# Performance work log

Hardware: AMD Instinct MI355X
Metric: run time of the kernel (lower is better)

The kernel has to match this reference:

```python
import jax, jax.numpy as jnp
import numpy as np

NEG = -1.0e9


def setup_inputs() -> dict:
    key = jax.random.key(0)
    ks = jax.random.split(key, 8)
    B, L, D = 4, 2048, 1024
    s = 1.0 / np.sqrt(D)
    return {
        "x": jax.random.normal(ks[0], (B, L, D), dtype=jnp.float32),
        "Wq": jax.random.normal(ks[1], (D, D), dtype=jnp.float32) * s,
        "bq": jax.random.normal(ks[2], (D,), dtype=jnp.float32) * 0.02,
        "Wk": jax.random.normal(ks[3], (D, D), dtype=jnp.float32) * s,
        "bk": jax.random.normal(ks[4], (D,), dtype=jnp.float32) * 0.02,
        "Wv": jax.random.normal(ks[5], (D, D), dtype=jnp.float32) * s,
        "bv": jax.random.normal(ks[6], (D,), dtype=jnp.float32) * 0.02,
        "lengths": jax.random.randint(ks[7], (B,), 1, 2048, dtype=jnp.int32),
    }


def reference(x, Wq, bq, Wk, bk, Wv, bv, lengths):
    # x: [B, L, D]; single-head self-attention with causal + length additive masks
    B, L, D = x.shape
    q = x @ Wq + bq  # [B, L, D]
    k = x @ Wk + bk
    v = x @ Wv + bv
    scale = 1.0 / jnp.sqrt(jnp.asarray(D, dtype=x.dtype))
    att = jnp.einsum("bid,bjd->bij", q, k) * scale  # [B, L, L]
    idx = jnp.arange(L)
    causal = jnp.where(idx[None, :] > idx[:, None], NEG, 0.0).astype(x.dtype)  # [L, L]
    # length mask: NEG where j >= len[b] or i >= len[b]
    invalid = (idx[None, :] >= lengths[:, None])  # [B, L]
    lenmask = jnp.where(invalid[:, :, None] | invalid[:, None, :], NEG, 0.0).astype(x.dtype)
    att = att + causal[None, :, :] + lenmask
    att = jax.nn.softmax(att, axis=-1)
    return jnp.einsum("bij,bjd->bid", att, v)
```

## Files before the change

kernel.cpp:

```cpp
#include <hip/hip_runtime.h>

#define NEGV (-1.0e9f)

typedef __bf16 bf16_t;
typedef __bf16 bf16x8 __attribute__((ext_vector_type(8)));
typedef __bf16 bf16x4 __attribute__((ext_vector_type(4)));
typedef float  f32x4  __attribute__((ext_vector_type(4)));

__device__ __forceinline__ void gld16(const void* g, void* l) {
    __builtin_amdgcn_global_load_lds(
        (const __attribute__((address_space(1))) void*)g,
        (__attribute__((address_space(3))) void*)l, 16, 0, 0);
}


#define STG(P0, P1, BASE, NB, HOFS) do {               \
    gld16(P0, (BASE) + (NB) * 32768 + (HOFS));         \
    gld16(P1, (BASE) + (NB) * 32768 + (HOFS) + 8192);  \
    P0 += 64; P1 += 64; } while (0)

#define MMROW(ai)                                                                                    \
    acc[ib + ai][0] = __builtin_amdgcn_mfma_f32_16x16x32_bf16(a##ai, b0, acc[ib + ai][0], 0, 0, 0);  \
    acc[ib + ai][1] = __builtin_amdgcn_mfma_f32_16x16x32_bf16(a##ai, b1, acc[ib + ai][1], 0, 0, 0);  \
    acc[ib + ai][2] = __builtin_amdgcn_mfma_f32_16x16x32_bf16(a##ai, b2, acc[ib + ai][2], 0, 0, 0);  \
    acc[ib + ai][3] = __builtin_amdgcn_mfma_f32_16x16x32_bf16(a##ai, b3, acc[ib + ai][3], 0, 0, 0)

#define PHASE(BUFO, HOFS, PK, STAGE_STMT, ENDW) do {                     \
    bf16x8 a0 = *(const bf16x8*)(rdA + (BUFO) + (HOFS)        + (PK));   \
    bf16x8 a1 = *(const bf16x8*)(rdA + (BUFO) + (HOFS) + 2048 + (PK));   \
    bf16x8 a2 = *(const bf16x8*)(rdA + (BUFO) + (HOFS) + 4096 + (PK));   \
    bf16x8 a3 = *(const bf16x8*)(rdA + (BUFO) + (HOFS) + 6144 + (PK));   \
    bf16x8 b0 = *(const bf16x8*)(rdB + (BUFO)          + (PK));          \
    bf16x8 b1 = *(const bf16x8*)(rdB + (BUFO) + 2048   + (PK));          \
    bf16x8 b2 = *(const bf16x8*)(rdB + (BUFO) + 4096   + (PK));          \
    bf16x8 b3 = *(const bf16x8*)(rdB + (BUFO) + 6144   + (PK));          \
    STAGE_STMT;                                                          \
    __builtin_amdgcn_s_barrier();                                        \
    asm volatile("s_waitcnt lgkmcnt(0)" ::: "memory");                   \
    __builtin_amdgcn_s_setprio(1);                                       \
    {                                                                    \
        const int ib = (HOFS) ? 4 : 0;                                   \
        MMROW(0); MMROW(1); MMROW(2); MMROW(3);                          \
    }                                                                    \
    __builtin_amdgcn_s_setprio(0);                                       \
    ENDW;                                                                \
    __builtin_amdgcn_s_barrier();                                        \
} while (0)

__device__ __forceinline__ void mainloop256(
    const bf16_t* __restrict__ A, const bf16_t* __restrict__ B,
    int ldA, int ldB, int nkt, char* smem, int tid, f32x4 acc[8][4])
{
    const int w    = tid >> 6;
    const int lane = tid & 63;
    const int wm   = w & 1;
    const int wn   = w >> 1;
    const int l16  = lane & 15;
    const int quad = lane >> 4;

    const int r0 = tid >> 3;
    const int c0 = ((tid & 7) ^ (r0 & 7)) * 8;
    const int s1 = 512 + tid;
    const int r1 = s1 >> 3;
    const int c1 = ((s1 & 7) ^ (r1 & 7)) * 8;

    const bf16_t* pa00 = A + (size_t)(r0)       * ldA + c0;
    const bf16_t* pa01 = A + (size_t)(r1)       * ldA + c1;
    const bf16_t* pa10 = A + (size_t)(128 + r0) * ldA + c0;
    const bf16_t* pa11 = A + (size_t)(128 + r1) * ldA + c1;
    const bf16_t* pb00 = B + (size_t)(r0)       * ldB + c0;
    const bf16_t* pb01 = B + (size_t)(r1)       * ldB + c1;
    const bf16_t* pb10 = B + (size_t)(128 + r0) * ldB + c0;
    const bf16_t* pb11 = B + (size_t)(128 + r1) * ldB + c1;

    char* const stA = smem + (w << 10);
    char* const stB = smem + 65536 + (w << 10);

    const int pk0 = ((quad    ) ^ (l16 & 7)) << 4;
    const int pk1 = ((quad + 4) ^ (l16 & 7)) << 4;
    const char* rdA = smem +         ((wm << 7) + l16) * 128;
    const char* rdB = smem + 65536 + ((wn << 6) + l16) * 128;

    STG(pa00, pa01, stA, 0, 0);
    STG(pa10, pa11, stA, 0, 16384);
    STG(pb00, pb01, stB, 0, 0);
    STG(pb10, pb11, stB, 0, 16384);
    asm volatile("s_waitcnt vmcnt(0)" ::: "memory");
    __builtin_amdgcn_s_barrier();

    for (int kt = 0; kt < nkt; ++kt) {
        const int bufo = (kt & 1) << 15;
        const int nb   = (kt & 1) ^ 1;
        const bool st  = (kt + 1) < nkt;
        PHASE(bufo, 0,    pk0, if (st) STG(pa00, pa01, stA, nb, 0),     );
        PHASE(bufo, 0,    pk1, if (st) STG(pa10, pa11, stA, nb, 16384), );
        PHASE(bufo, 8192, pk0, if (st) STG(pb00, pb01, stB, nb, 0),     );
        PHASE(bufo, 8192, pk1, if (st) STG(pb10, pb11, stB, nb, 16384),
              asm volatile("s_waitcnt vmcnt(0)" ::: "memory"));
    }
}


#define STG2(P0, P1, DST) do {                                   \
    gld16(P0, (DST)); gld16(P1, (char*)(DST) + 8192);            \
    P0 += 64; P1 += 64; } while (0)

#define MM2ROW(ai)                                                                         \
    acc[ai][0] = __builtin_amdgcn_mfma_f32_16x16x32_bf16(a##ai, b0, acc[ai][0], 0, 0, 0);  \
    acc[ai][1] = __builtin_amdgcn_mfma_f32_16x16x32_bf16(a##ai, b1, acc[ai][1], 0, 0, 0);  \
    acc[ai][2] = __builtin_amdgcn_mfma_f32_16x16x32_bf16(a##ai, b2, acc[ai][2], 0, 0, 0);  \
    acc[ai][3] = __builtin_amdgcn_mfma_f32_16x16x32_bf16(a##ai, b3, acc[ai][3], 0, 0, 0)

#define PHASEX(AOFS, BOFS, PK, STAGE_STMT, ENDW) do {                  \
    bf16x8 a0 = *(const bf16x8*)(rdA + (AOFS)        + (PK));          \
    bf16x8 a1 = *(const bf16x8*)(rdA + (AOFS) + 2048 + (PK));          \
    bf16x8 a2 = *(const bf16x8*)(rdA + (AOFS) + 4096 + (PK));          \
    bf16x8 a3 = *(const bf16x8*)(rdA + (AOFS) + 6144 + (PK));          \
    bf16x8 b0 = *(const bf16x8*)(rdB + (BOFS)        + (PK));          \
    bf16x8 b1 = *(const bf16x8*)(rdB + (BOFS) + 2048 + (PK));          \
    bf16x8 b2 = *(const bf16x8*)(rdB + (BOFS) + 4096 + (PK));          \
    bf16x8 b3 = *(const bf16x8*)(rdB + (BOFS) + 6144 + (PK));          \
    STAGE_STMT;                                                        \
    __builtin_amdgcn_s_barrier();                                      \
    asm volatile("s_waitcnt lgkmcnt(0)" ::: "memory");                 \
    __builtin_amdgcn_s_setprio(1);                                     \
    MM2ROW(0); MM2ROW(1); MM2ROW(2); MM2ROW(3);                        \
    __builtin_amdgcn_s_setprio(0);                                     \
    ENDW;                                                              \
    __builtin_amdgcn_s_barrier();                                      \
} while (0)

__device__ __forceinline__ void mainloop256x128(
    const bf16_t* __restrict__ A, const bf16_t* __restrict__ B,
    int ldA, int ldB, int nkt, char* smem, int tid, f32x4 acc[4][4])
{
    const int w    = tid >> 6;
    const int lane = tid & 63;
    const int wm   = w & 3;
    const int wn   = w >> 2;
    const int l16  = lane & 15;
    const int quad = lane >> 4;

    const int r0 = tid >> 3;
    const int c0 = ((tid & 7) ^ (r0 & 7)) * 8;
    const int s1 = 512 + tid;
    const int r1 = s1 >> 3;
    const int c1 = ((s1 & 7) ^ (r1 & 7)) * 8;

    const bf16_t* pa00 = A + (size_t)(r0)       * ldA + c0;
    const bf16_t* pa01 = A + (size_t)(r1)       * ldA + c1;
    const bf16_t* pa10 = A + (size_t)(128 + r0) * ldA + c0;
    const bf16_t* pa11 = A + (size_t)(128 + r1) * ldA + c1;
    const bf16_t* pb0  = B + (size_t)(r0)       * ldB + c0;
    const bf16_t* pb1  = B + (size_t)(r1)       * ldB + c1;

    char* const stA = smem + (w << 10);
    char* const stB = smem + 65536 + (w << 10);

    const int pk0 = ((quad    ) ^ (l16 & 7)) << 4;
    const int pk1 = ((quad + 4) ^ (l16 & 7)) << 4;
    const char* rdA = smem +         ((wm << 6) + l16) * 128;
    const char* rdB = smem + 65536 + ((wn << 6) + l16) * 128;

    STG2(pa00, pa01, stA);
    STG2(pa10, pa11, stA + 16384);
    STG2(pb0,  pb1,  stB);
    asm volatile("s_waitcnt vmcnt(0)" ::: "memory");
    __builtin_amdgcn_s_barrier();

    for (int kt = 0; kt < nkt; ++kt) {
        const int aofs = (kt & 1) << 15;
        const int bofs = (kt & 1) << 14;
        char* const nA = stA + ((((kt & 1) ^ 1)) << 15);
        char* const nB = stB + ((((kt & 1) ^ 1)) << 14);
        const bool st  = (kt + 1) < nkt;
        PHASEX(aofs, bofs, pk0,
               if (st) { STG2(pa00, pa01, nA); STG2(pa10, pa11, nA + 16384); }, );
        PHASEX(aofs, bofs, pk1,
               if (st) { STG2(pb0, pb1, nB); },
               asm volatile("s_waitcnt vmcnt(0)" ::: "memory"));
    }
}

__global__ __launch_bounds__(256)
void convert_x_kernel(const float* __restrict__ x, bf16_t* __restrict__ xb)
{
    const size_t i = ((size_t)blockIdx.x * 256 + threadIdx.x) * 8;
    float4 a = *(const float4*)&x[i];
    float4 b = *(const float4*)&x[i + 4];
    bf16x8 o;
    o[0] = (bf16_t)a.x; o[1] = (bf16_t)a.y; o[2] = (bf16_t)a.z; o[3] = (bf16_t)a.w;
    o[4] = (bf16_t)b.x; o[5] = (bf16_t)b.y; o[6] = (bf16_t)b.z; o[7] = (bf16_t)b.w;
    *(bf16x8*)&xb[i] = o;
}

__global__ __launch_bounds__(256)
void transpose_w_kernel(const float* __restrict__ W0, const float* __restrict__ W1,
                        const float* __restrict__ W2, bf16_t* __restrict__ WT)
{
    __shared__ float t[32][33];
    const float* W = (blockIdx.z == 0) ? W0 : (blockIdx.z == 1) ? W1 : W2;
    bf16_t* WTz = WT + (size_t)blockIdx.z * 1024 * 1024;
    const int k0 = blockIdx.y * 32, n0 = blockIdx.x * 32;
    const int r = threadIdx.x >> 3, c4 = (threadIdx.x & 7) * 4;
    float4 v = *(const float4*)&W[(size_t)(k0 + r) * 1024 + n0 + c4];
    t[r][c4 + 0] = v.x; t[r][c4 + 1] = v.y; t[r][c4 + 2] = v.z; t[r][c4 + 3] = v.w;
    __syncthreads();
    bf16x4 o;
#pragma unroll
    for (int j = 0; j < 4; ++j) o[j] = (bf16_t)t[c4 + j][r];
    *(bf16x4*)&WTz[(size_t)(n0 + r) * 1024 + k0 + c4] = o;
}

__global__ __launch_bounds__(512, 2)
void gemm_qk256(const bf16_t* __restrict__ A, const bf16_t* __restrict__ Bt,
                const float* __restrict__ bq, const float* __restrict__ bk,
                bf16_t* __restrict__ C, int N, int Kd)
{
    __shared__ __align__(16) char smem[131072];
    int bid = blockIdx.y * 8 + blockIdx.x;
    bid = (bid & 7) * 32 + (bid >> 3);
    const int n0 = (bid & 7) * 256;
    const int m0 = (bid >> 3) * 256;
    const int tid = threadIdx.x;

    f32x4 acc[8][4];
#pragma unroll
    for (int i = 0; i < 8; ++i)
#pragma unroll
        for (int j = 0; j < 4; ++j) acc[i][j] = (f32x4)(0.0f);

    mainloop256(A + (size_t)m0 * Kd, Bt + (size_t)n0 * Kd, Kd, Kd, Kd >> 6,
                smem, tid, acc);

    const int w = tid >> 6, lane = tid & 63;
    const int wm = w & 1, wn = w >> 1, quad = lane >> 4, l16 = lane & 15;
#pragma unroll
    for (int j = 0; j < 4; ++j) {
        const int col = n0 + wn * 64 + j * 16 + l16;
        const float bval = (col < 1024) ? bq[col] : bk[col - 1024];
#pragma unroll
        for (int i = 0; i < 8; ++i) {
            const int row = m0 + wm * 128 + i * 16 + quad * 4;
#pragma unroll
            for (int r = 0; r < 4; ++r)
                C[(size_t)(row + r) * N + col] = (bf16_t)(acc[i][j][r] + bval);
        }
    }
}

__global__ __launch_bounds__(512, 2)
void gemm_vt256(const bf16_t* __restrict__ WvT, const bf16_t* __restrict__ xb,
                const float* __restrict__ bv, bf16_t* __restrict__ VT,
                int N, int Kd)
{
    __shared__ __align__(16) char smem[98304];
    const int m0 = blockIdx.y * 256;
    const int n0 = blockIdx.x * 128;
    const int tid = threadIdx.x;

    f32x4 acc[4][4];
#pragma unroll
    for (int i = 0; i < 4; ++i)
#pragma unroll
        for (int j = 0; j < 4; ++j) acc[i][j] = (f32x4)(0.0f);

    mainloop256x128(WvT + (size_t)m0 * Kd, xb + (size_t)n0 * Kd, Kd, Kd, Kd >> 6,
                    smem, tid, acc);

    const int w = tid >> 6, lane = tid & 63;
    const int wm = w & 3, wn = w >> 2, quad = lane >> 4, l16 = lane & 15;
#pragma unroll
    for (int i = 0; i < 4; ++i) {
        const int row = m0 + wm * 64 + i * 16 + quad * 4;
#pragma unroll
        for (int r = 0; r < 4; ++r) {
            const float bval = bv[row + r];
#pragma unroll
            for (int j = 0; j < 4; ++j) {
                const int col = n0 + wn * 64 + j * 16 + l16;
                VT[(size_t)(row + r) * N + col] = (bf16_t)(acc[i][j][r] + bval);
            }
        }
    }
}

__global__ __launch_bounds__(512, 2)
void scores256(const bf16_t* __restrict__ Q, const bf16_t* __restrict__ K,
               int ldq, const int* __restrict__ lengths,
               float* __restrict__ S, int L, int Dd, float alpha)
{
    __shared__ __align__(16) char smem[98304];
    const int b = blockIdx.z;
    const int len = lengths[b];
    int mt = 0;
    while ((mt + 1) * (mt + 2) <= (int)blockIdx.x) ++mt;
    const int jt = blockIdx.x - mt * (mt + 1);
    const int m0 = mt * 256, n0 = jt * 128;
    float* Sb = S + (size_t)b * L * L;
    const int tid = threadIdx.x;

    f32x4 acc[4][4];
#pragma unroll
    for (int i = 0; i < 4; ++i)
#pragma unroll
        for (int j = 0; j < 4; ++j) acc[i][j] = (f32x4)(0.0f);

    const bf16_t* Qb = Q + (size_t)b * L * ldq + (size_t)m0 * ldq;
    const bf16_t* Kb = K + (size_t)b * L * ldq + (size_t)n0 * ldq;
    mainloop256x128(Qb, Kb, ldq, ldq, Dd >> 6, smem, tid, acc);

    const int w = tid >> 6, lane = tid & 63;
    const int wm = w & 3, wn = w >> 2, quad = lane >> 4, l16 = lane & 15;
#pragma unroll
    for (int i = 0; i < 4; ++i) {
#pragma unroll
        for (int j = 0; j < 4; ++j) {
            const int col = n0 + wn * 64 + j * 16 + l16;
#pragma unroll
            for (int r = 0; r < 4; ++r) {
                const int row = m0 + wm * 64 + i * 16 + quad * 4 + r;
                float s = acc[i][j][r] * alpha;
                if (col > row) s += NEGV;
                if (row >= len || col >= len) s += NEGV;
                Sb[(size_t)row * L + col] = s;
            }
        }
    }
}

__global__ __launch_bounds__(256)
void softmax_kernel(const float* __restrict__ S, bf16_t* __restrict__ P,
                    int L, int ldp)
{
    __shared__ float red[8];
    const int i = blockIdx.x;
    const int bound  = ((i >> 7) + 1) << 7;
    const int bound2 = ((i >> 8) + 1) << 8;
    const float* row = S + ((size_t)blockIdx.y * L + i) * L;
    bf16_t* prow = P + ((size_t)blockIdx.y * L + i) * ldp;
    const int t = threadIdx.x;
    const int w = t >> 6, lane = t & 63;
    const int j8 = t * 8;
    const bool act = j8 < bound;

    float v[8];
    float m = -3.0e38f;
    if (act) {
        float4 a = *(const float4*)&row[j8];
        float4 b = *(const float4*)&row[j8 + 4];
        v[0] = a.x; v[1] = a.y; v[2] = a.z; v[3] = a.w;
        v[4] = b.x; v[5] = b.y; v[6] = b.z; v[7] = b.w;
#pragma unroll
        for (int j = 0; j < 8; ++j) m = fmaxf(m, v[j]);
    }
#pragma unroll
    for (int off = 32; off > 0; off >>= 1) m = fmaxf(m, __shfl_down(m, off, 64));
    if (lane == 0) red[w] = m;
    __syncthreads();
    m = fmaxf(fmaxf(red[0], red[1]), fmaxf(red[2], red[3]));

    float s = 0.f;
    if (act) {
#pragma unroll
        for (int j = 0; j < 8; ++j) {
            v[j] = __expf(v[j] - m);
            s += v[j];
        }
    }
#pragma unroll
    for (int off = 32; off > 0; off >>= 1) s += __shfl_down(s, off, 64);
    if (lane == 0) red[4 + w] = s;
    __syncthreads();
    s = red[4] + red[5] + red[6] + red[7];

    if (act) {
        const float inv = 1.0f / s;
        bf16x8 o;
#pragma unroll
        for (int j = 0; j < 8; ++j) o[j] = (bf16_t)(v[j] * inv);
        *(bf16x8*)&prow[j8] = o;
    } else if (j8 < bound2) {
        bf16x8 z;
#pragma unroll
        for (int j = 0; j < 8; ++j) z[j] = (bf16_t)0.0f;
        *(bf16x8*)&prow[j8] = z;
    }
}

__global__ __launch_bounds__(512, 2)
void pv256(const bf16_t* __restrict__ P, int ldp,
           const bf16_t* __restrict__ VT, int ldv,
           float* __restrict__ O, int L, int Dd)
{
    __shared__ __align__(16) char smem[98304];
    const int b = blockIdx.z;
    const int mt = gridDim.y - 1 - blockIdx.y;
    const int m0 = mt * 256, n0 = blockIdx.x * 128;
    const int tid = threadIdx.x;

    f32x4 acc[4][4];
#pragma unroll
    for (int i = 0; i < 4; ++i)
#pragma unroll
        for (int j = 0; j < 4; ++j) acc[i][j] = (f32x4)(0.0f);

    const int nkt = (m0 + 256) >> 6;
    const bf16_t* Pb = P + (size_t)b * L * ldp + (size_t)m0 * ldp;
    const bf16_t* Vb = VT + (size_t)b * L + (size_t)n0 * ldv;
    mainloop256x128(Pb, Vb, ldp, ldv, nkt, smem, tid, acc);

    float* Ob = O + (size_t)b * L * Dd;
    const int w = tid >> 6, lane = tid & 63;
    const int wm = w & 3, wn = w >> 2, quad = lane >> 4, l16 = lane & 15;
#pragma unroll
    for (int i = 0; i < 4; ++i) {
        const int row = m0 + wm * 64 + i * 16 + quad * 4;
#pragma unroll
        for (int j = 0; j < 4; ++j) {
            const int col = n0 + wn * 64 + j * 16 + l16;
#pragma unroll
            for (int r = 0; r < 4; ++r)
                Ob[(size_t)(row + r) * Dd + col] = acc[i][j][r];
        }
    }
}

extern "C" void kernel_launch(void* const* d_in, const int* in_sizes, int n_in,
                              void* d_out, int out_size, void* d_ws, size_t ws_size,
                              hipStream_t stream)
{
    const float* x  = (const float*)d_in[0];
    const float* Wq = (const float*)d_in[1];
    const float* bq = (const float*)d_in[2];
    const float* Wk = (const float*)d_in[3];
    const float* bk = (const float*)d_in[4];
    const float* Wv = (const float*)d_in[5];
    const float* bv = (const float*)d_in[6];
    const int*  len = (const int*)d_in[7];
    float* out = (float*)d_out;

    const int B = 4, L = 2048, D = 1024;
    const int M = B * L;
    const int N2 = 2 * D;

    bf16_t* xb = (bf16_t*)d_ws;
    bf16_t* WT = xb + (size_t)M * D;
    bf16_t* QK = WT + (size_t)3 * D * D;
    bf16_t* VT = QK + (size_t)M * N2;
    float*  S  = (float*)(VT + (size_t)D * M);
    bf16_t* P  = QK;

    convert_x_kernel<<<(M * D) / 2048, 256, 0, stream>>>(x, xb);

    transpose_w_kernel<<<dim3(32, 32, 3), 256, 0, stream>>>(Wq, Wk, Wv, WT);

    gemm_qk256<<<dim3(8, 32), 512, 0, stream>>>(xb, WT, bq, bk, QK, N2, D);

    gemm_vt256<<<dim3(64, 4), 512, 0, stream>>>(
        WT + (size_t)2 * D * D, xb, bv, VT, M, D);

    scores256<<<dim3(72, 1, B), 512, 0, stream>>>(
        QK, QK + 1024, N2, len, S, L, D, 0.03125f);

    softmax_kernel<<<dim3(L, B), 256, 0, stream>>>(S, P, L, N2);

    pv256<<<dim3(8, 8, 4), 512, 0, stream>>>(P, N2, VT, M, out, L, D);
}
```

Measured before the change: 259.9 us.

## Issue all next-tile loads up front and remap block indices for XCD locality

The GEMM main loops now issue every global-to-LDS prefetch for the next K tile in the first phase instead of spreading them across phases, so memory latency has more compute to hide behind. The block indices of the V-projection, scores and PV kernels are also permuted so that consecutive hardware block IDs, which are dealt round-robin across the 8 XCDs, map to neighbouring tiles that share operand rows and columns in each XCD's L2. The remapping hardcodes grid sizes (64, 8, 72 tiles) and only works for these fixed shapes. Issuing all loads at once may raise VMEM queue pressure.

```diff
diff --git a/kernel.cpp b/kernel.cpp
--- a/kernel.cpp
+++ b/kernel.cpp
@@ -92,10 +92,14 @@
         const int bufo = (kt & 1) << 15;
         const int nb   = (kt & 1) ^ 1;
         const bool st  = (kt + 1) < nkt;
-        PHASE(bufo, 0,    pk0, if (st) STG(pa00, pa01, stA, nb, 0),     );
-        PHASE(bufo, 0,    pk1, if (st) STG(pa10, pa11, stA, nb, 16384), );
-        PHASE(bufo, 8192, pk0, if (st) STG(pb00, pb01, stB, nb, 0),     );
-        PHASE(bufo, 8192, pk1, if (st) STG(pb10, pb11, stB, nb, 16384),
+        PHASE(bufo, 0,    pk0,
+              if (st) { STG(pa00, pa01, stA, nb, 0);
+                        STG(pa10, pa11, stA, nb, 16384);
+                        STG(pb00, pb01, stB, nb, 0);
+                        STG(pb10, pb11, stB, nb, 16384); }, );
+        PHASE(bufo, 0,    pk1, , );
+        PHASE(bufo, 8192, pk0, , );
+        PHASE(bufo, 8192, pk1, ,
               asm volatile("s_waitcnt vmcnt(0)" ::: "memory"));
     }
 }
@@ -175,9 +179,10 @@
         char* const nB = stB + ((((kt & 1) ^ 1)) << 14);
         const bool st  = (kt + 1) < nkt;
         PHASEX(aofs, bofs, pk0,
-               if (st) { STG2(pa00, pa01, nA); STG2(pa10, pa11, nA + 16384); }, );
-        PHASEX(aofs, bofs, pk1,
-               if (st) { STG2(pb0, pb1, nB); },
+               if (st) { STG2(pa00, pa01, nA);
+                         STG2(pa10, pa11, nA + 16384);
+                         STG2(pb0, pb1, nB); }, );
+        PHASEX(aofs, bofs, pk1, ,
                asm volatile("s_waitcnt vmcnt(0)" ::: "memory"));
     }
 }
@@ -255,8 +260,10 @@
                 int N, int Kd)
 {
     __shared__ __align__(16) char smem[98304];
-    const int m0 = blockIdx.y * 256;
-    const int n0 = blockIdx.x * 128;
+    int bid = blockIdx.y * 64 + blockIdx.x;
+    bid = (bid & 7) * 32 + (bid >> 3);
+    const int m0 = (bid >> 6) * 256;
+    const int n0 = (bid & 63) * 128;
     const int tid = threadIdx.x;
 
     f32x4 acc[4][4];
@@ -293,9 +300,11 @@
     __shared__ __align__(16) char smem[98304];
     const int b = blockIdx.z;
     const int len = lengths[b];
+    int tix = (int)blockIdx.x;
+    tix = (tix & 7) * 9 + (tix >> 3);
     int mt = 0;
-    while ((mt + 1) * (mt + 2) <= (int)blockIdx.x) ++mt;
-    const int jt = blockIdx.x - mt * (mt + 1);
+    while ((mt + 1) * (mt + 2) <= tix) ++mt;
+    const int jt = tix - mt * (mt + 1);
     const int m0 = mt * 256, n0 = jt * 128;
     float* Sb = S + (size_t)b * L * L;
     const int tid = threadIdx.x;
@@ -395,8 +404,10 @@
 {
     __shared__ __align__(16) char smem[98304];
     const int b = blockIdx.z;
-    const int mt = gridDim.y - 1 - blockIdx.y;
-    const int m0 = mt * 256, n0 = blockIdx.x * 128;
+    int bid = blockIdx.y * 8 + blockIdx.x;
+    bid = (bid & 7) * 8 + (bid >> 3);
+    const int mt = 7 - (bid >> 3);
+    const int m0 = mt * 256, n0 = (bid & 7) * 128;
     const int tid = threadIdx.x;
 
     f32x4 acc[4][4];
```

After: 253.1 us. -2.6%, faster.
